# Optimization experiments

Measured on AMD Instinct MI355X. Metric: run time of the kernel, lower is better.

## Reference

```python
import jax, jax.numpy as jnp
import numpy as np

TEMPERATURE = 0.02
B, T, D = 32, 256, 128


def _l2norm(x):
    return x / jnp.linalg.norm(x, axis=-1, keepdims=True)


def setup_inputs() -> dict:
    key = jax.random.key(0)
    k1, k2, k3, k4, k5, k6 = jax.random.split(key, 6)
    query_single = _l2norm(jax.random.normal(k1, (B, D), dtype=jnp.float32))
    pos_single = _l2norm(jax.random.normal(k2, (B, D), dtype=jnp.float32))
    query_multi = _l2norm(jax.random.normal(k3, (B, T, D), dtype=jnp.float32))
    pos_multi = _l2norm(jax.random.normal(k4, (B, T, D), dtype=jnp.float32))
    # variable-length masks (at least 1 valid token each, like real tokenized batches)
    q_len = jax.random.randint(k5, (B,), T // 4, T + 1)
    p_len = jax.random.randint(k6, (B,), T // 4, T + 1)
    pos = jnp.arange(T)[None, :]
    q_mask = pos < q_len[:, None]
    p_mask = pos < p_len[:, None]
    return {
        "query_single": query_single,
        "pos_single": pos_single,
        "query_multi": query_multi,
        "pos_multi": pos_multi,
        "q_mask": q_mask,
        "p_mask": p_mask,
    }


def _late_interaction_similarity(q_tokens, q_mask, p_tokens, p_mask):
    # All-pairs token similarity: [Bq, Bp, Tq, Tp]
    sim = jnp.einsum("bqd,cpd->bcqp", q_tokens, p_tokens)
    neg = jnp.finfo(sim.dtype).min
    sim = jnp.where(p_mask[None, :, None, :], sim, neg)
    mx = jnp.max(sim, axis=-1)                       # [Bq, Bp, Tq]
    mx = jnp.where(q_mask[:, None, :], mx, 0.0)      # drop invalid query tokens
    s = jnp.sum(mx, axis=-1)                         # [Bq, Bp]
    t_i = jnp.maximum(jnp.sum(q_mask, axis=-1), 1).astype(sim.dtype)  # [Bq]
    return s / t_i[:, None]


def _diag_cross_entropy(logits):
    # labels = arange(B): standard in-batch InfoNCE
    logp = jax.nn.log_softmax(logits, axis=-1)
    return -jnp.mean(jnp.diagonal(logp))


def reference(query_single, pos_single, query_multi, pos_multi, q_mask, p_mask):
    tau = TEMPERATURE
    dense_sim = query_single @ pos_single.T                       # [B, B]
    single_loss = _diag_cross_entropy(dense_sim / tau)

    S_late = _late_interaction_similarity(query_multi, q_mask, pos_multi, p_mask)
    multi_loss = _diag_cross_entropy(S_late / tau)

    dense_probs = jax.nn.softmax(dense_sim / tau, axis=1)
    late_probs = jax.nn.softmax(S_late / tau, axis=1)
    eps = 1e-8
    kl = jnp.mean(jnp.sum(dense_probs * jnp.log((dense_probs + eps) / (late_probs + eps)), axis=1))

    total_loss = single_loss + multi_loss + kl
    return (total_loss, single_loss, multi_loss, kl)
```

## Files before the change

### kernel.cpp

```cpp
#include <hip/hip_runtime.h>
#include <hip/hip_bf16.h>

#define B_SZ 32
#define T_SZ 256
#define D_SZ 128
#define TAU_INV 50.0f

typedef __bf16 bf16x8 __attribute__((ext_vector_type(8)));
typedef float f32x4 __attribute__((ext_vector_type(4)));

__device__ __forceinline__ bool mask_is_byte(const void* m) {
    return ((const int*)m)[0] != 1;
}
__device__ __forceinline__ int mget(const void* m, int idx, bool isb) {
    return isb ? (((const unsigned char*)m)[idx] != 0) : (((const int*)m)[idx] != 0);
}

__device__ __forceinline__ bf16x8 cvt8(float4 a, float4 b) {
    union { bf16x8 v; __hip_bfloat16 h[8]; } u;
    u.h[0] = __float2bfloat16(a.x); u.h[1] = __float2bfloat16(a.y);
    u.h[2] = __float2bfloat16(a.z); u.h[3] = __float2bfloat16(a.w);
    u.h[4] = __float2bfloat16(b.x); u.h[5] = __float2bfloat16(b.y);
    u.h[6] = __float2bfloat16(b.z); u.h[7] = __float2bfloat16(b.w);
    return u.v;
}

__global__ __launch_bounds__(512, 4) void fused(
    const float* __restrict__ qs,  const float* __restrict__ ps,
    const float* __restrict__ qm3, const float* __restrict__ pm3,
    const void* __restrict__ qmask, const void* __restrict__ pmask,
    float* __restrict__ sraw, unsigned int* __restrict__ counter,
    float* __restrict__ out)
{
    __shared__ __align__(16) unsigned char Plds[T_SZ * D_SZ * 2];
    __shared__ float madd[T_SZ];
    __shared__ float qmul[2][T_SZ];
    __shared__ float wsum[2][8];
    __shared__ int lastflag;

    const int tid = threadIdx.x;
    const int l   = tid & 63;
    const int w   = tid >> 6;
    const int bid = blockIdx.x;
    const int c   = bid & 31;
    const int bg  = bid >> 5;
    const int b0  = bg, b1 = bg + 16;
    const int lr  = l & 15;
    const int lg  = l >> 4;

    const bool isb = mask_is_byte(qmask);

    int p_hi;
    {
        int v = 0;
        #pragma unroll
        for (int j = 0; j < 4; ++j)
            if (mget(pmask, c * T_SZ + l * 4 + j, isb)) v = l * 4 + j + 1;
        #pragma unroll
        for (int off = 1; off < 64; off <<= 1) {
            int o = __shfl_xor(v, off);
            v = v > o ? v : o;
        }
        p_hi = v > 1 ? v : 1;
    }
    const int ptmax   = (p_hi + 15) >> 4;
    const int stiters = (p_hi + 31) >> 5;

    const int qrow = w * 32 + (l & 31);
    const bool do0 = __any(mget(qmask, b0 * T_SZ + qrow, isb));
    const bool do1 = __any(mget(qmask, b1 * T_SZ + qrow, isb));

    {
        const float4* Pc4 = (const float4*)(pm3 + c * (T_SZ * D_SZ));
        for (int it = 0; it < stiters; ++it) {
            int m   = it * 512 + tid;
            int row = m >> 4;
            int cs  = m & 15;
            float4 a = Pc4[m * 2], b = Pc4[m * 2 + 1];
            *(bf16x8*)(Plds + row * 256 + ((cs ^ (row & 7)) << 4)) = cvt8(a, b);
        }
    }
    {
        int t = tid & 255;
        if (tid < 256) madd[t] = mget(pmask, c * T_SZ + t, isb) ? 0.0f : -1e30f;
        qmul[tid >> 8][t] = mget(qmask, (tid < 256 ? b0 : b1) * T_SZ + t, isb) ? 1.0f : 0.0f;
    }

    bf16x8 qf0[2][4] = {}, qf1[2][4] = {};
    if (do0)
        #pragma unroll
        for (int qt = 0; qt < 2; ++qt)
            #pragma unroll
            for (int k = 0; k < 4; ++k) {
                const float4* s = (const float4*)(qm3 + b0 * (T_SZ * D_SZ)
                                   + (w * 32 + qt * 16 + lr) * D_SZ + k * 32 + lg * 8);
                qf0[qt][k] = cvt8(s[0], s[1]);
            }
    if (do1)
        #pragma unroll
        for (int qt = 0; qt < 2; ++qt)
            #pragma unroll
            for (int k = 0; k < 4; ++k) {
                const float4* s = (const float4*)(qm3 + b1 * (T_SZ * D_SZ)
                                   + (w * 32 + qt * 16 + lr) * D_SZ + k * 32 + lg * 8);
                qf1[qt][k] = cvt8(s[0], s[1]);
            }

    __syncthreads();

    float r00 = -3e38f, r01 = -3e38f, r10 = -3e38f, r11 = -3e38f;

    for (int pt = 0; pt < ptmax; ++pt) {
        f32x4 a00 = {0,0,0,0}, a01 = {0,0,0,0}, a10 = {0,0,0,0}, a11 = {0,0,0,0};
        #pragma unroll
        for (int k = 0; k < 4; ++k) {
            int row = pt * 16 + lr;
            bf16x8 af = *(const bf16x8*)(Plds + row * 256 + (((k * 4 + lg) ^ (row & 7)) << 4));
            if (do0) {
                a00 = __builtin_amdgcn_mfma_f32_16x16x32_bf16(af, qf0[0][k], a00, 0, 0, 0);
                a01 = __builtin_amdgcn_mfma_f32_16x16x32_bf16(af, qf0[1][k], a01, 0, 0, 0);
            }
            if (do1) {
                a10 = __builtin_amdgcn_mfma_f32_16x16x32_bf16(af, qf1[0][k], a10, 0, 0, 0);
                a11 = __builtin_amdgcn_mfma_f32_16x16x32_bf16(af, qf1[1][k], a11, 0, 0, 0);
            }
        }
        float pm0 = madd[pt * 16 + lg * 4 + 0];
        float pm1 = madd[pt * 16 + lg * 4 + 1];
        float pm2 = madd[pt * 16 + lg * 4 + 2];
        float pm3v = madd[pt * 16 + lg * 4 + 3];
        if (do0) {
            r00 = fmaxf(r00, fmaxf(fmaxf(a00[0]+pm0, a00[1]+pm1), fmaxf(a00[2]+pm2, a00[3]+pm3v)));
            r01 = fmaxf(r01, fmaxf(fmaxf(a01[0]+pm0, a01[1]+pm1), fmaxf(a01[2]+pm2, a01[3]+pm3v)));
        }
        if (do1) {
            r10 = fmaxf(r10, fmaxf(fmaxf(a10[0]+pm0, a10[1]+pm1), fmaxf(a10[2]+pm2, a10[3]+pm3v)));
            r11 = fmaxf(r11, fmaxf(fmaxf(a11[0]+pm0, a11[1]+pm1), fmaxf(a11[2]+pm2, a11[3]+pm3v)));
        }
    }

    r00 = fmaxf(r00, __shfl_xor(r00, 16)); r00 = fmaxf(r00, __shfl_xor(r00, 32));
    r01 = fmaxf(r01, __shfl_xor(r01, 16)); r01 = fmaxf(r01, __shfl_xor(r01, 32));
    r10 = fmaxf(r10, __shfl_xor(r10, 16)); r10 = fmaxf(r10, __shfl_xor(r10, 32));
    r11 = fmaxf(r11, __shfl_xor(r11, 16)); r11 = fmaxf(r11, __shfl_xor(r11, 32));

    float t0 = r00 * qmul[0][w * 32 + lr] + r01 * qmul[0][w * 32 + 16 + lr];
    float t1 = r10 * qmul[1][w * 32 + lr] + r11 * qmul[1][w * 32 + 16 + lr];
    #pragma unroll
    for (int off = 32; off > 0; off >>= 1) {
        t0 += __shfl_down(t0, off);
        t1 += __shfl_down(t1, off);
    }
    if (l == 0) { wsum[0][w] = t0 * 0.25f; wsum[1][w] = t1 * 0.25f; }
    __syncthreads();

    if (tid == 0) {
        float s0 = 0.f, s1 = 0.f;
        #pragma unroll
        for (int ww = 0; ww < 8; ++ww) { s0 += wsum[0][ww]; s1 += wsum[1][ww]; }
        sraw[b0 * 32 + c] = s0;
        sraw[b1 * 32 + c] = s1;
        __threadfence();
        unsigned int old = atomicAdd(counter, 1u);
        lastflag = (old == (unsigned int)(gridDim.x - 1));
    }
    __syncthreads();
    if (!lastflag) return;

    __threadfence();

    float* qsL   = (float*)Plds;
    float* psL   = qsL + 32 * 132;
    float* dense = psL + 32 * 132;
    float* late  = dense + 32 * 32;
    float* tcnt  = late + 32 * 32;
    float* rsA   = tcnt + 32;
    float* rmA   = rsA + 32;
    float* rkA   = rmA + 32;

    for (int i = tid; i < 1024; i += 512) {
        int r = i >> 5, c4 = (i & 31) * 4;
        *(float4*)(qsL + r * 132 + c4) = *(const float4*)(qs + r * D_SZ + c4);
        *(float4*)(psL + r * 132 + c4) = *(const float4*)(ps + r * D_SZ + c4);
    }
    if (tid < 256) {
        const int r = tid >> 3, j = tid & 7;
        int cnt = 0;
        if (isb) {
            const unsigned int* mm = (const unsigned int*)((const unsigned char*)qmask + r * T_SZ + j * 32);
            #pragma unroll
            for (int t = 0; t < 8; ++t) cnt += (int)((mm[t] * 0x01010101u) >> 24);
        } else {
            const int* mm = (const int*)qmask + r * T_SZ + j * 32;
            #pragma unroll
            for (int t = 0; t < 32; ++t) cnt += (mm[t] != 0);
        }
        cnt += __shfl_xor(cnt, 1);
        cnt += __shfl_xor(cnt, 2);
        cnt += __shfl_xor(cnt, 4);
        if (j == 0) tcnt[r] = (float)(cnt > 1 ? cnt : 1);
    }
    __syncthreads();

    for (int idx = tid; idx < B_SZ * B_SZ; idx += 512) {
        int r = idx >> 5, cc = idx & 31;
        float s = 0.f;
        #pragma unroll
        for (int i = 0; i < D_SZ; i += 4) {
            float4 a  = *(const float4*)(qsL + r  * 132 + i);
            float4 bb = *(const float4*)(psL + cc * 132 + i);
            s += a.x * bb.x + a.y * bb.y + a.z * bb.z + a.w * bb.w;
        }
        dense[r * 32 + cc] = s;
        late[r * 32 + cc]  = sraw[idx] / tcnt[r];
    }
    __syncthreads();

    {
        const int cc = tid & 31;
        #pragma unroll
        for (int it = 0; it < 2; ++it) {
            const int r = (tid >> 5) + 16 * it;
            float xd = dense[r * 32 + cc] * TAU_INV;
            float xl = late[r * 32 + cc]  * TAU_INV;
            float md = xd, ml = xl;
            #pragma unroll
            for (int off = 16; off > 0; off >>= 1) {
                md = fmaxf(md, __shfl_xor(md, off));
                ml = fmaxf(ml, __shfl_xor(ml, off));
            }
            float sd = expf(xd - md), sl = expf(xl - ml);
            #pragma unroll
            for (int off = 16; off > 0; off >>= 1) {
                sd += __shfl_xor(sd, off);
                sl += __shfl_xor(sl, off);
            }
            float lsd = md + logf(sd);
            float lsl = ml + logf(sl);
            float pd = expf(xd - lsd);
            float pl = expf(xl - lsl);
            float klt = pd * logf((pd + 1e-8f) / (pl + 1e-8f));
            #pragma unroll
            for (int off = 16; off > 0; off >>= 1) klt += __shfl_xor(klt, off);
            if (cc == 0) rkA[r] = klt;
            if (cc == r) { rsA[r] = -(xd - lsd); rmA[r] = -(xl - lsl); }
        }
    }
    __syncthreads();

    if (tid < B_SZ) {
        float a = rsA[tid], bb = rmA[tid], c2 = rkA[tid];
        #pragma unroll
        for (int off = 16; off > 0; off >>= 1) {
            a  += __shfl_xor(a, off);
            bb += __shfl_xor(bb, off);
            c2 += __shfl_xor(c2, off);
        }
        if (tid == 0) {
            a *= (1.0f / B_SZ); bb *= (1.0f / B_SZ); c2 *= (1.0f / B_SZ);
            out[0] = a + bb + c2;
            out[1] = a;
            out[2] = bb;
            out[3] = c2;
        }
    }
}

extern "C" void kernel_launch(void* const* d_in, const int* in_sizes, int n_in,
                              void* d_out, int out_size, void* d_ws, size_t ws_size,
                              hipStream_t stream) {
    const float* qs    = (const float*)d_in[0];
    const float* ps    = (const float*)d_in[1];
    const float* qm3   = (const float*)d_in[2];
    const float* pm3   = (const float*)d_in[3];
    const void*  qmask = d_in[4];
    const void*  pmask = d_in[5];
    float* out = (float*)d_out;

    float* sraw = (float*)d_ws;
    unsigned int* counter = (unsigned int*)((char*)d_ws + 4096);

    hipMemsetAsync(counter, 0, sizeof(unsigned int), stream);
    fused<<<512, 512, 0, stream>>>(qs, ps, qm3, pm3, qmask, pmask,
                                   sraw, counter, out);
}
```

Measured before the change: 42.76 us.

## Process two passage docs per 1024-thread block with register-prefetched second tile

```diff
diff --git a/kernel.cpp b/kernel.cpp
--- a/kernel.cpp
+++ b/kernel.cpp
@@ -25,117 +25,145 @@
     return u.v;
 }
 
-__global__ __launch_bounds__(512, 4) void fused(
+__global__ __launch_bounds__(1024, 4) void uber(
     const float* __restrict__ qs,  const float* __restrict__ ps,
     const float* __restrict__ qm3, const float* __restrict__ pm3,
     const void* __restrict__ qmask, const void* __restrict__ pmask,
     float* __restrict__ sraw, unsigned int* __restrict__ counter,
     float* __restrict__ out)
 {
-    __shared__ __align__(16) unsigned char Plds[T_SZ * D_SZ * 2];
-    __shared__ float madd[T_SZ];
-    __shared__ float qmul[2][T_SZ];
-    __shared__ float wsum[2][8];
+    __shared__ __align__(16) unsigned char Pl[2][T_SZ * D_SZ * 2];
+    __shared__ float maddL[2][T_SZ];
+    __shared__ float qmulL[2][T_SZ];
+    __shared__ float wsum[16][2];
     __shared__ int lastflag;
 
     const int tid = threadIdx.x;
     const int l   = tid & 63;
     const int w   = tid >> 6;
     const int bid = blockIdx.x;
-    const int c   = bid & 31;
-    const int bg  = bid >> 5;
+    const int xcd = bid & 7;
+    const int j   = bid >> 3;
+    const int bg  = xcd * 2 + (j >> 4);
+    const int cp  = j & 15;
+    const int c0  = cp * 2, c1 = cp * 2 + 1;
     const int b0  = bg, b1 = bg + 16;
     const int lr  = l & 15;
     const int lg  = l >> 4;
+    const int wb  = w >> 3;
+    const int myb = wb ? b1 : b0;
+    const int s   = (w & 7) * 32;
 
     const bool isb = mask_is_byte(qmask);
 
-    int p_hi;
-    {
-        int v = 0;
-        #pragma unroll
-        for (int j = 0; j < 4; ++j)
-            if (mget(pmask, c * T_SZ + l * 4 + j, isb)) v = l * 4 + j + 1;
+    int pt0, pt1;
+    {
+        int v0 = 0, v1 = 0;
+        #pragma unroll
+        for (int j2 = 0; j2 < 4; ++j2) {
+            int t = l * 4 + j2;
+            if (mget(pmask, c0 * T_SZ + t, isb)) v0 = t + 1;
+            if (mget(pmask, c1 * T_SZ + t, isb)) v1 = t + 1;
+        }
         #pragma unroll
         for (int off = 1; off < 64; off <<= 1) {
-            int o = __shfl_xor(v, off);
-            v = v > o ? v : o;
-        }
-        p_hi = v > 1 ? v : 1;
-    }
-    const int ptmax   = (p_hi + 15) >> 4;
-    const int stiters = (p_hi + 31) >> 5;
-
-    const int qrow = w * 32 + (l & 31);
-    const bool do0 = __any(mget(qmask, b0 * T_SZ + qrow, isb));
-    const bool do1 = __any(mget(qmask, b1 * T_SZ + qrow, isb));
-
-    {
-        const float4* Pc4 = (const float4*)(pm3 + c * (T_SZ * D_SZ));
-        for (int it = 0; it < stiters; ++it) {
-            int m   = it * 512 + tid;
-            int row = m >> 4;
-            int cs  = m & 15;
-            float4 a = Pc4[m * 2], b = Pc4[m * 2 + 1];
-            *(bf16x8*)(Plds + row * 256 + ((cs ^ (row & 7)) << 4)) = cvt8(a, b);
-        }
-    }
-    {
-        int t = tid & 255;
-        if (tid < 256) madd[t] = mget(pmask, c * T_SZ + t, isb) ? 0.0f : -1e30f;
-        qmul[tid >> 8][t] = mget(qmask, (tid < 256 ? b0 : b1) * T_SZ + t, isb) ? 1.0f : 0.0f;
-    }
-
-    bf16x8 qf0[2][4] = {}, qf1[2][4] = {};
-    if (do0)
+            int o0 = __shfl_xor(v0, off), o1 = __shfl_xor(v1, off);
+            v0 = o0 > v0 ? o0 : v0;
+            v1 = o1 > v1 ? o1 : v1;
+        }
+        pt0 = ((v0 > 1 ? v0 : 1) + 15) >> 4;
+        pt1 = ((v1 > 1 ? v1 : 1) + 15) >> 4;
+    }
+
+    const bool dob = __any(mget(qmask, myb * T_SZ + s + (l & 31), isb));
+
+    bf16x8 qf[2][4] = {};
+    if (dob)
         #pragma unroll
         for (int qt = 0; qt < 2; ++qt)
             #pragma unroll
             for (int k = 0; k < 4; ++k) {
-                const float4* s = (const float4*)(qm3 + b0 * (T_SZ * D_SZ)
-                                   + (w * 32 + qt * 16 + lr) * D_SZ + k * 32 + lg * 8);
-                qf0[qt][k] = cvt8(s[0], s[1]);
+                const float4* sp = (const float4*)(qm3 + myb * (T_SZ * D_SZ)
+                                    + (s + qt * 16 + lr) * D_SZ + k * 32 + lg * 8);
+                qf[qt][k] = cvt8(sp[0], sp[1]);
             }
-    if (do1)
-        #pragma unroll
-        for (int qt = 0; qt < 2; ++qt)
-            #pragma unroll
-            for (int k = 0; k < 4; ++k) {
-                const float4* s = (const float4*)(qm3 + b1 * (T_SZ * D_SZ)
-                                   + (w * 32 + qt * 16 + lr) * D_SZ + k * 32 + lg * 8);
-                qf1[qt][k] = cvt8(s[0], s[1]);
-            }
-
-    __syncthreads();
-
-    float r00 = -3e38f, r01 = -3e38f, r10 = -3e38f, r11 = -3e38f;
-
-    for (int pt = 0; pt < ptmax; ++pt) {
-        f32x4 a00 = {0,0,0,0}, a01 = {0,0,0,0}, a10 = {0,0,0,0}, a11 = {0,0,0,0};
+
+    {
+        const float4* Pc = (const float4*)(pm3 + c0 * (T_SZ * D_SZ));
+        #pragma unroll
+        for (int it = 0; it < 4; ++it) {
+            int m = it * 1024 + tid;
+            int row = m >> 4, cs = m & 15;
+            float4 a = Pc[m * 2], b = Pc[m * 2 + 1];
+            *(bf16x8*)(Pl[0] + row * 256 + ((cs ^ (row & 7)) << 4)) = cvt8(a, b);
+        }
+    }
+    {
+        int grp = tid >> 8, t = tid & 255;
+        if (grp == 0)      maddL[0][t] = mget(pmask, c0 * T_SZ + t, isb) ? 0.0f : -1e30f;
+        else if (grp == 1) maddL[1][t] = mget(pmask, c1 * T_SZ + t, isb) ? 0.0f : -1e30f;
+        else if (grp == 2) qmulL[0][t] = mget(qmask, b0 * T_SZ + t, isb) ? 1.0f : 0.0f;
+        else               qmulL[1][t] = mget(qmask, b1 * T_SZ + t, isb) ? 1.0f : 0.0f;
+    }
+    __syncthreads();
+
+    const float4* Pc1 = (const float4*)(pm3 + c1 * (T_SZ * D_SZ));
+    float4 e0 = Pc1[tid * 2],              f0 = Pc1[tid * 2 + 1];
+    float4 e1 = Pc1[(1024 + tid) * 2],     f1 = Pc1[(1024 + tid) * 2 + 1];
+    float4 e2 = Pc1[(2048 + tid) * 2],     f2 = Pc1[(2048 + tid) * 2 + 1];
+    float4 e3 = Pc1[(3072 + tid) * 2],     f3 = Pc1[(3072 + tid) * 2 + 1];
+
+    float r00 = -3e38f, r01 = -3e38f;
+    float r10 = -3e38f, r11 = -3e38f;
+
+    for (int pt = 0; pt < pt0; ++pt) {
+        f32x4 a0 = {0,0,0,0}, a1 = {0,0,0,0};
         #pragma unroll
         for (int k = 0; k < 4; ++k) {
             int row = pt * 16 + lr;
-            bf16x8 af = *(const bf16x8*)(Plds + row * 256 + (((k * 4 + lg) ^ (row & 7)) << 4));
-            if (do0) {
-                a00 = __builtin_amdgcn_mfma_f32_16x16x32_bf16(af, qf0[0][k], a00, 0, 0, 0);
-                a01 = __builtin_amdgcn_mfma_f32_16x16x32_bf16(af, qf0[1][k], a01, 0, 0, 0);
+            bf16x8 af = *(const bf16x8*)(Pl[0] + row * 256 + (((k * 4 + lg) ^ (row & 7)) << 4));
+            if (dob) {
+                a0 = __builtin_amdgcn_mfma_f32_16x16x32_bf16(af, qf[0][k], a0, 0, 0, 0);
+                a1 = __builtin_amdgcn_mfma_f32_16x16x32_bf16(af, qf[1][k], a1, 0, 0, 0);
             }
-            if (do1) {
-                a10 = __builtin_amdgcn_mfma_f32_16x16x32_bf16(af, qf1[0][k], a10, 0, 0, 0);
-                a11 = __builtin_amdgcn_mfma_f32_16x16x32_bf16(af, qf1[1][k], a11, 0, 0, 0);
+        }
+        float pm0 = maddL[0][pt * 16 + lg * 4 + 0];
+        float pm1 = maddL[0][pt * 16 + lg * 4 + 1];
+        float pm2 = maddL[0][pt * 16 + lg * 4 + 2];
+        float pm3v = maddL[0][pt * 16 + lg * 4 + 3];
+        if (dob) {
+            r00 = fmaxf(r00, fmaxf(fmaxf(a0[0]+pm0, a0[1]+pm1), fmaxf(a0[2]+pm2, a0[3]+pm3v)));
+            r01 = fmaxf(r01, fmaxf(fmaxf(a1[0]+pm0, a1[1]+pm1), fmaxf(a1[2]+pm2, a1[3]+pm3v)));
+        }
+    }
+
+    {
+        int m0 = tid, m1 = 1024 + tid, m2 = 2048 + tid, m3 = 3072 + tid;
+        *(bf16x8*)(Pl[1] + (m0 >> 4) * 256 + (((m0 & 15) ^ ((m0 >> 4) & 7)) << 4)) = cvt8(e0, f0);
+        *(bf16x8*)(Pl[1] + (m1 >> 4) * 256 + (((m1 & 15) ^ ((m1 >> 4) & 7)) << 4)) = cvt8(e1, f1);
+        *(bf16x8*)(Pl[1] + (m2 >> 4) * 256 + (((m2 & 15) ^ ((m2 >> 4) & 7)) << 4)) = cvt8(e2, f2);
+        *(bf16x8*)(Pl[1] + (m3 >> 4) * 256 + (((m3 & 15) ^ ((m3 >> 4) & 7)) << 4)) = cvt8(e3, f3);
+    }
+    __syncthreads();
+
+    for (int pt = 0; pt < pt1; ++pt) {
+        f32x4 a0 = {0,0,0,0}, a1 = {0,0,0,0};
+        #pragma unroll
+        for (int k = 0; k < 4; ++k) {
+            int row = pt * 16 + lr;
+            bf16x8 af = *(const bf16x8*)(Pl[1] + row * 256 + (((k * 4 + lg) ^ (row & 7)) << 4));
+            if (dob) {
+                a0 = __builtin_amdgcn_mfma_f32_16x16x32_bf16(af, qf[0][k], a0, 0, 0, 0);
+                a1 = __builtin_amdgcn_mfma_f32_16x16x32_bf16(af, qf[1][k], a1, 0, 0, 0);
             }
         }
-        float pm0 = madd[pt * 16 + lg * 4 + 0];
-        float pm1 = madd[pt * 16 + lg * 4 + 1];
-        float pm2 = madd[pt * 16 + lg * 4 + 2];
-        float pm3v = madd[pt * 16 + lg * 4 + 3];
-        if (do0) {
-            r00 = fmaxf(r00, fmaxf(fmaxf(a00[0]+pm0, a00[1]+pm1), fmaxf(a00[2]+pm2, a00[3]+pm3v)));
-            r01 = fmaxf(r01, fmaxf(fmaxf(a01[0]+pm0, a01[1]+pm1), fmaxf(a01[2]+pm2, a01[3]+pm3v)));
-        }
-        if (do1) {
-            r10 = fmaxf(r10, fmaxf(fmaxf(a10[0]+pm0, a10[1]+pm1), fmaxf(a10[2]+pm2, a10[3]+pm3v)));
-            r11 = fmaxf(r11, fmaxf(fmaxf(a11[0]+pm0, a11[1]+pm1), fmaxf(a11[2]+pm2, a11[3]+pm3v)));
+        float pm0 = maddL[1][pt * 16 + lg * 4 + 0];
+        float pm1 = maddL[1][pt * 16 + lg * 4 + 1];
+        float pm2 = maddL[1][pt * 16 + lg * 4 + 2];
+        float pm3v = maddL[1][pt * 16 + lg * 4 + 3];
+        if (dob) {
+            r10 = fmaxf(r10, fmaxf(fmaxf(a0[0]+pm0, a0[1]+pm1), fmaxf(a0[2]+pm2, a0[3]+pm3v)));
+            r11 = fmaxf(r11, fmaxf(fmaxf(a1[0]+pm0, a1[1]+pm1), fmaxf(a1[2]+pm2, a1[3]+pm3v)));
         }
     }
 
@@ -144,23 +172,26 @@
     r10 = fmaxf(r10, __shfl_xor(r10, 16)); r10 = fmaxf(r10, __shfl_xor(r10, 32));
     r11 = fmaxf(r11, __shfl_xor(r11, 16)); r11 = fmaxf(r11, __shfl_xor(r11, 32));
 
-    float t0 = r00 * qmul[0][w * 32 + lr] + r01 * qmul[0][w * 32 + 16 + lr];
-    float t1 = r10 * qmul[1][w * 32 + lr] + r11 * qmul[1][w * 32 + 16 + lr];
+    float t0 = r00 * qmulL[wb][s + lr] + r01 * qmulL[wb][s + 16 + lr];
+    float t1 = r10 * qmulL[wb][s + lr] + r11 * qmulL[wb][s + 16 + lr];
     #pragma unroll
     for (int off = 32; off > 0; off >>= 1) {
         t0 += __shfl_down(t0, off);
         t1 += __shfl_down(t1, off);
     }
-    if (l == 0) { wsum[0][w] = t0 * 0.25f; wsum[1][w] = t1 * 0.25f; }
-    __syncthreads();
-
+    if (l == 0) { wsum[w][0] = t0 * 0.25f; wsum[w][1] = t1 * 0.25f; }
+    __syncthreads();
+
+    if (tid < 4) {
+        const int bsel = tid >> 1, csel = tid & 1;
+        float sum = 0.f;
+        #pragma unroll
+        for (int ww = 0; ww < 8; ++ww) sum += wsum[bsel * 8 + ww][csel];
+        sraw[(bsel ? b1 : b0) * 32 + (csel ? c1 : c0)] = sum;
+    }
+    __threadfence();
+    __syncthreads();
     if (tid == 0) {
-        float s0 = 0.f, s1 = 0.f;
-        #pragma unroll
-        for (int ww = 0; ww < 8; ++ww) { s0 += wsum[0][ww]; s1 += wsum[1][ww]; }
-        sraw[b0 * 32 + c] = s0;
-        sraw[b1 * 32 + c] = s1;
-        __threadfence();
         unsigned int old = atomicAdd(counter, 1u);
         lastflag = (old == (unsigned int)(gridDim.x - 1));
     }
@@ -169,86 +200,81 @@
 
     __threadfence();
 
-    float* qsL   = (float*)Plds;
-    float* psL   = qsL + 32 * 132;
-    float* dense = psL + 32 * 132;
-    float* late  = dense + 32 * 32;
-    float* tcnt  = late + 32 * 32;
-    float* rsA   = tcnt + 32;
-    float* rmA   = rsA + 32;
-    float* rkA   = rmA + 32;
-
-    for (int i = tid; i < 1024; i += 512) {
-        int r = i >> 5, c4 = (i & 31) * 4;
-        *(float4*)(qsL + r * 132 + c4) = *(const float4*)(qs + r * D_SZ + c4);
-        *(float4*)(psL + r * 132 + c4) = *(const float4*)(ps + r * D_SZ + c4);
-    }
-    if (tid < 256) {
-        const int r = tid >> 3, j = tid & 7;
+    float* base   = (float*)Pl;
+    float* denseA = base;
+    float* lateA  = base + 1024;
+    float* tcntL  = base + 2048;
+    float* rsA    = base + 2080;
+    float* rmA    = rsA + 32;
+    float* rkA    = rmA + 32;
+
+    {
+        const int h = l >> 5, lane32 = l & 31;
+        const int r = w * 2 + h;
         int cnt = 0;
-        if (isb) {
-            const unsigned int* mm = (const unsigned int*)((const unsigned char*)qmask + r * T_SZ + j * 32);
-            #pragma unroll
-            for (int t = 0; t < 8; ++t) cnt += (int)((mm[t] * 0x01010101u) >> 24);
-        } else {
-            const int* mm = (const int*)qmask + r * T_SZ + j * 32;
-            #pragma unroll
-            for (int t = 0; t < 32; ++t) cnt += (mm[t] != 0);
-        }
-        cnt += __shfl_xor(cnt, 1);
-        cnt += __shfl_xor(cnt, 2);
-        cnt += __shfl_xor(cnt, 4);
-        if (j == 0) tcnt[r] = (float)(cnt > 1 ? cnt : 1);
-    }
-    __syncthreads();
-
-    for (int idx = tid; idx < B_SZ * B_SZ; idx += 512) {
-        int r = idx >> 5, cc = idx & 31;
-        float s = 0.f;
-        #pragma unroll
-        for (int i = 0; i < D_SZ; i += 4) {
-            float4 a  = *(const float4*)(qsL + r  * 132 + i);
-            float4 bb = *(const float4*)(psL + cc * 132 + i);
-            s += a.x * bb.x + a.y * bb.y + a.z * bb.z + a.w * bb.w;
-        }
-        dense[r * 32 + cc] = s;
-        late[r * 32 + cc]  = sraw[idx] / tcnt[r];
-    }
-    __syncthreads();
-
-    {
-        const int cc = tid & 31;
-        #pragma unroll
-        for (int it = 0; it < 2; ++it) {
-            const int r = (tid >> 5) + 16 * it;
-            float xd = dense[r * 32 + cc] * TAU_INV;
-            float xl = late[r * 32 + cc]  * TAU_INV;
-            float md = xd, ml = xl;
-            #pragma unroll
-            for (int off = 16; off > 0; off >>= 1) {
-                md = fmaxf(md, __shfl_xor(md, off));
-                ml = fmaxf(ml, __shfl_xor(ml, off));
-            }
-            float sd = expf(xd - md), sl = expf(xl - ml);
-            #pragma unroll
-            for (int off = 16; off > 0; off >>= 1) {
-                sd += __shfl_xor(sd, off);
-                sl += __shfl_xor(sl, off);
-            }
-            float lsd = md + logf(sd);
-            float lsl = ml + logf(sl);
-            float pd = expf(xd - lsd);
-            float pl = expf(xl - lsl);
-            float klt = pd * logf((pd + 1e-8f) / (pl + 1e-8f));
-            #pragma unroll
-            for (int off = 16; off > 0; off >>= 1) klt += __shfl_xor(klt, off);
-            if (cc == 0) rkA[r] = klt;
-            if (cc == r) { rsA[r] = -(xd - lsd); rmA[r] = -(xl - lsl); }
-        }
-    }
-    __syncthreads();
-
-    if (tid < B_SZ) {
+        #pragma unroll
+        for (int k = 0; k < 8; ++k)
+            cnt += mget(qmask, r * T_SZ + lane32 + k * 32, isb);
+        #pragma unroll
+        for (int off = 1; off < 32; off <<= 1) cnt += __shfl_xor(cnt, off);
+        if (lane32 == 0) tcntL[r] = (float)(cnt > 1 ? cnt : 1);
+    }
+    __syncthreads();
+
+    {
+        const int r = tid >> 5, cc = tid & 31;
+        const float4* qa = (const float4*)(qs + r  * D_SZ);
+        const float4* pb = (const float4*)(ps + cc * D_SZ);
+        float sdot = 0.f;
+        #pragma unroll
+        for (int i = 0; i < 32; ++i) {
+            float4 a = qa[i], b = pb[i];
+            sdot += a.x * b.x + a.y * b.y + a.z * b.z + a.w * b.w;
+        }
+        denseA[tid] = sdot;
+        lateA[tid]  = sraw[tid] / tcntL[r];
+    }
+    __syncthreads();
+
+    {
+        const int h = l >> 5, lane32 = l & 31;
+        const int r = w * 2 + h;
+        float xd = denseA[r * 32 + lane32] * TAU_INV;
+        float xl = lateA[r * 32 + lane32]  * TAU_INV;
+        float md = xd, ml = xl;
+        #pragma unroll
+        for (int off = 16; off > 0; off >>= 1) {
+            md = fmaxf(md, __shfl_xor(md, off));
+            ml = fmaxf(ml, __shfl_xor(ml, off));
+        }
+        float sd = expf(xd - md), sl = expf(xl - ml);
+        #pragma unroll
+        for (int off = 16; off > 0; off >>= 1) {
+            sd += __shfl_xor(sd, off);
+            sl += __shfl_xor(sl, off);
+        }
+        float lsd = md + logf(sd);
+        float lsl = ml + logf(sl);
+        float pd = expf(xd - lsd);
+        float pl = expf(xl - lsl);
+        float klt = pd * logf((pd + 1e-8f) / (pl + 1e-8f));
+        #pragma unroll
+        for (int off = 16; off > 0; off >>= 1) klt += __shfl_xor(klt, off);
+
+        float logpd = xd - lsd;
+        float logpl = xl - lsl;
+        int srcLane = (l & 32) + r;
+        float dlogd = __shfl(logpd, srcLane);
+        float dlogl = __shfl(logpl, srcLane);
+        if (lane32 == 0) {
+            rsA[r] = -dlogd;
+            rmA[r] = -dlogl;
+            rkA[r] = klt;
+        }
+    }
+    __syncthreads();
+
+    if (tid < 32) {
         float a = rsA[tid], bb = rmA[tid], c2 = rkA[tid];
         #pragma unroll
         for (int off = 16; off > 0; off >>= 1) {
@@ -281,6 +307,6 @@
     unsigned int* counter = (unsigned int*)((char*)d_ws + 4096);
 
     hipMemsetAsync(counter, 0, sizeof(unsigned int), stream);
-    fused<<<512, 512, 0, stream>>>(qs, ps, qm3, pm3, qmask, pmask,
+    uber<<<256, 1024, 0, stream>>>(qs, ps, qm3, pm3, qmask, pmask,
                                    sraw, counter, out);
 }
```

Result: slower. 116.5 us (+172.4%).
